# Performance work log

Hardware: AMD Instinct MI355X
Metric: run time of the kernel (lower is better)

## Reference

```python
import jax, jax.numpy as jnp
import numpy as np

B, N, D, K = 2, 8192, 512, 16


def setup_inputs() -> dict:
    key = jax.random.key(0)
    k1, k2, k3, k4 = jax.random.split(key, 4)
    x = jax.random.normal(k1, (B, N, D), dtype=jnp.float32)
    xyz = jax.random.normal(k2, (B, N, 3), dtype=jnp.float32)
    # nn.Linear(d_model, 3*d_model): weight [3D, D], bias [3D]
    W_qkv = jax.random.normal(k3, (3 * D, D), dtype=jnp.float32) * 0.02
    b_qkv = jnp.zeros((3 * D,), dtype=jnp.float32)
    # nn.Linear(d_model, d_model)
    W_fc = jax.random.normal(k4, (D, D), dtype=jnp.float32) * 0.02
    b_fc = jnp.zeros((D,), dtype=jnp.float32)
    return {"x": x, "xyz": xyz, "W_qkv": W_qkv, "b_qkv": b_qkv, "W_fc": W_fc, "b_fc": b_fc}


def _knn_idx(xyz):
    # squared-distance KNN (same ordering as cdist): |a|^2 + |b|^2 - 2 a.b
    sq = jnp.sum(xyz * xyz, axis=-1)                      # [B, N]
    d2 = sq[:, :, None] + sq[:, None, :] - 2.0 * jnp.einsum('bnc,bmc->bnm', xyz, xyz)
    return jax.lax.top_k(-d2, K)[1]                       # [B, N, K] smallest distances


def reference(x, xyz, W_qkv, b_qkv, W_fc, b_fc):
    knn_idx = _knn_idx(xyz)                               # no-grad in original
    qkv = jnp.einsum('bnd,ed->bne', x, W_qkv) + b_qkv     # [B, N, 3D]
    qkv = qkv.reshape(B, N, 3, D)
    q, k, v = qkv[:, :, 0], qkv[:, :, 1], qkv[:, :, 2]    # [B, N, D]
    gather = jax.vmap(lambda arr, idx: arr[idx])          # per-batch neighbor gather
    k_neigh = gather(k, knn_idx)                          # [B, N, K, D]
    v_neigh = gather(v, knn_idx)                          # [B, N, K, D]
    # faithful to einsum('bnd,bnsk->bns', q, k_neigh): sums d and feature dims independently
    attn = (q.sum(-1)[:, :, None] * k_neigh.sum(-1)) / jnp.sqrt(jnp.float32(D))  # [B, N, K]
    attn = jax.nn.softmax(attn, axis=2)[..., None]        # [B, N, K, 1]
    x_out = (attn * v_neigh).sum(axis=2)                  # [B, N, D]
    return jnp.einsum('bnd,ed->bne', x_out, W_fc) + b_fc + x
```

## Files before the change

kernel.cpp:

```cpp
#include <hip/hip_runtime.h>

typedef _Float16 half_t;
typedef _Float16 half8 __attribute__((ext_vector_type(8)));
typedef _Float16 half4v __attribute__((ext_vector_type(4)));
typedef float f32x4 __attribute__((ext_vector_type(4)));

#define NB 2
#define NN 8192
#define ND 512
#define NKNN 16
#define BN (NB*NN)

#define OFF_XH   0ull
#define OFF_VH   (OFF_XH  + (size_t)BN*ND*2)
#define OFF_XOH  (OFF_VH  + (size_t)BN*ND*2)
#define OFF_WVH  (OFF_XOH + (size_t)BN*ND*2)
#define OFF_WFCH (OFF_WVH + (size_t)ND*ND*2)
#define OFF_XW   (OFF_WFCH+ (size_t)ND*ND*2)
#define OFF_IDX  (OFF_XW  + (size_t)BN*16)
#define OFF_WQC  (OFF_IDX + (size_t)BN*NKNN*4)
#define OFF_WKC  (OFF_WQC + 2048)
#define OFF_QKB  (OFF_WKC + 2048)
#define OFF_QS   (OFF_QKB + 256)
#define OFF_KS   (OFF_QS  + (size_t)BN*4)

__global__ __launch_bounds__(256) void kcolsum(const float* __restrict__ W,
                                               float* __restrict__ wq,
                                               float* __restrict__ wk) {
  int h = blockIdx.x >> 3, g = blockIdx.x & 7;
  int t = threadIdx.x, dl = t & 63, s = t >> 6;
  const float* Wb = W + (size_t)h * 512 * 512;
  int d = g * 64 + dl;
  float acc = 0.f;
  for (int e = s * 128; e < s * 128 + 128; ++e) acc += Wb[(size_t)e * 512 + d];
  __shared__ float red[4][64];
  red[s][dl] = acc;
  __syncthreads();
  if (s == 0) (h ? wk : wq)[d] = red[0][dl] + red[1][dl] + red[2][dl] + red[3][dl];
}

__global__ __launch_bounds__(512) void kbias(const float* __restrict__ b,
                                             float* __restrict__ qkb) {
  __shared__ float r0[512], r1[512];
  int t = threadIdx.x;
  r0[t] = b[t]; r1[t] = b[512 + t];
  __syncthreads();
  for (int s = 256; s; s >>= 1) {
    if (t < s) { r0[t] += r0[t + s]; r1[t] += r1[t + s]; }
    __syncthreads();
  }
  if (t == 0) { qkb[0] = r0[0]; qkb[1] = r1[0]; }
}

__global__ __launch_bounds__(256) void kconvw(const float* __restrict__ wqkv,
                                              const float* __restrict__ wfc,
                                              half_t* __restrict__ wvh,
                                              half_t* __restrict__ wfch) {
  int i = blockIdx.x * 256 + threadIdx.x;
  float4 a = ((const float4*)(wqkv + 1024 * 512))[i];
  half4v ha; ha[0]=(half_t)a.x; ha[1]=(half_t)a.y; ha[2]=(half_t)a.z; ha[3]=(half_t)a.w;
  *(half4v*)(wvh + (size_t)i * 4) = ha;
  float4 c = ((const float4*)wfc)[i];
  half4v hc; hc[0]=(half_t)c.x; hc[1]=(half_t)c.y; hc[2]=(half_t)c.z; hc[3]=(half_t)c.w;
  *(half4v*)(wfch + (size_t)i * 4) = hc;
}

__global__ __launch_bounds__(256) void kxh(const float* __restrict__ x,
                                           const float* __restrict__ wq,
                                           const float* __restrict__ wk,
                                           const float* __restrict__ qkb,
                                           half_t* __restrict__ xh,
                                           float* __restrict__ qs,
                                           float* __restrict__ ks) {
  int wid = blockIdx.x * 4 + (threadIdx.x >> 6);
  int l = threadIdx.x & 63;
  size_t base = (size_t)wid * ND + l * 8;
  float4 a0 = *(const float4*)(x + base);
  float4 a1 = *(const float4*)(x + base + 4);
  half8 h;
  h[0]=(half_t)a0.x; h[1]=(half_t)a0.y; h[2]=(half_t)a0.z; h[3]=(half_t)a0.w;
  h[4]=(half_t)a1.x; h[5]=(half_t)a1.y; h[6]=(half_t)a1.z; h[7]=(half_t)a1.w;
  *(half8*)(xh + base) = h;
  float4 q0 = ((const float4*)(wq + l * 8))[0], q1 = ((const float4*)(wq + l * 8))[1];
  float4 k0 = ((const float4*)(wk + l * 8))[0], k1 = ((const float4*)(wk + l * 8))[1];
  float dq = a0.x*q0.x + a0.y*q0.y + a0.z*q0.z + a0.w*q0.w
           + a1.x*q1.x + a1.y*q1.y + a1.z*q1.z + a1.w*q1.w;
  float dk = a0.x*k0.x + a0.y*k0.y + a0.z*k0.z + a0.w*k0.w
           + a1.x*k1.x + a1.y*k1.y + a1.z*k1.z + a1.w*k1.w;
  #pragma unroll
  for (int o = 32; o; o >>= 1) { dq += __shfl_xor(dq, o); dk += __shfl_xor(dk, o); }
  if (l == 0) { qs[wid] = dq + qkb[0]; ks[wid] = dk + qkb[1]; }
}

__global__ __launch_bounds__(256) void kxyzw(const float* __restrict__ xyz,
                                             float4* __restrict__ xw) {
  int i = blockIdx.x * 256 + threadIdx.x;
  float ax = xyz[(size_t)i * 3 + 0], ay = xyz[(size_t)i * 3 + 1], az = xyz[(size_t)i * 3 + 2];
  float sq = __fadd_rn(__fadd_rn(__fmul_rn(ax, ax), __fmul_rn(ay, ay)), __fmul_rn(az, az));
  xw[i] = make_float4(ax, ay, az, sq);
}

#define QPW 4
__global__ __launch_bounds__(256) void kknn(const float4* __restrict__ xw,
                                            int* __restrict__ idxo) {
  __shared__ float4 tile[1024];
  const int tid = threadIdx.x;
  const int l = tid & 63;
  const int w = tid >> 6;
  const int b = blockIdx.x >> 9;
  const int qbase = (blockIdx.x & 511) * (4 * QPW) + w * QPW;
  const float4* xb = xw + (size_t)b * NN;

  float4 qp[QPW];
  #pragma unroll
  for (int qi = 0; qi < QPW; ++qi) qp[qi] = xb[qbase + qi];

  float mind[QPW]; int mini[QPW];
  #pragma unroll
  for (int qi = 0; qi < QPW; ++qi) { mind[qi] = __builtin_inff(); mini[qi] = 0x7fffffff; }

  for (int t = 0; t < 8; ++t) {
    __syncthreads();
    #pragma unroll
    for (int i = 0; i < 4; ++i) tile[i * 256 + tid] = xb[t * 1024 + i * 256 + tid];
    __syncthreads();
    #pragma unroll 4
    for (int it = 0; it < 16; ++it) {
      float4 cp = tile[it * 64 + l];
      int ci = t * 1024 + it * 64 + l;
      #pragma unroll
      for (int qi = 0; qi < QPW; ++qi) {
        float dot = fmaf(qp[qi].z, cp.z, fmaf(qp[qi].y, cp.y, __fmul_rn(qp[qi].x, cp.x)));
        float d2 = __fsub_rn(__fadd_rn(qp[qi].w, cp.w), __fmul_rn(2.0f, dot));
        if (d2 < mind[qi]) { mind[qi] = d2; mini[qi] = ci; }
      }
    }
  }

  float kd[QPW]; int ki[QPW]; float wst[QPW];
  #pragma unroll
  for (int qi = 0; qi < QPW; ++qi) {
    float d = mind[qi]; int ii = mini[qi];
    #pragma unroll
    for (int k = 2; k <= 64; k <<= 1) {
      #pragma unroll
      for (int j = k >> 1; j > 0; j >>= 1) {
        float od = __shfl_xor(d, j);
        int   oi = __shfl_xor(ii, j);
        bool up = ((l & k) == 0);
        bool lower_lane = ((l & j) == 0);
        bool oless = (od < d) || (od == d && oi < ii);
        bool take = (up == lower_lane) ? oless : !oless;
        if (take) { d = od; ii = oi; }
      }
    }
    kd[qi] = __shfl(d, l & 15);
    ki[qi] = __shfl(ii, l & 15);
    wst[qi] = __shfl(d, 15);
  }

  for (int t = 0; t < 8; ++t) {
    __syncthreads();
    #pragma unroll
    for (int i = 0; i < 4; ++i) tile[i * 256 + tid] = xb[t * 1024 + i * 256 + tid];
    __syncthreads();
    #pragma unroll 2
    for (int it = 0; it < 16; ++it) {
      float4 cp = tile[it * 64 + l];
      int ci = t * 1024 + it * 64 + l;
      #pragma unroll
      for (int qi = 0; qi < QPW; ++qi) {
        float dot = fmaf(qp[qi].z, cp.z, fmaf(qp[qi].y, cp.y, __fmul_rn(qp[qi].x, cp.x)));
        float d2 = __fsub_rn(__fadd_rn(qp[qi].w, cp.w), __fmul_rn(2.0f, dot));
        bool ok = (d2 <= wst[qi]) && (ci != mini[qi]);
        unsigned long long m = __ballot(ok);
        while (m) {
          int a = __builtin_ctzll(m);
          m &= m - 1;
          float dc = __shfl(d2, a);
          int ic = __shfl(ci, a);
          bool lower = (kd[qi] < dc) || (kd[qi] == dc && ki[qi] < ic);
          int r = __popcll(__ballot(lower) & 0xFFFFull);
          if (r < 16) {
            float pd = __shfl_up(kd[qi], 1, 16);
            int pi = __shfl_up(ki[qi], 1, 16);
            int p = l & 15;
            if (p == r)      { kd[qi] = dc; ki[qi] = ic; }
            else if (p > r)  { kd[qi] = pd; ki[qi] = pi; }
            wst[qi] = __shfl(kd[qi], 15, 16);
          }
        }
      }
    }
  }

  if (l < 16) {
    #pragma unroll
    for (int qi = 0; qi < QPW; ++qi)
      idxo[((size_t)b * NN + qbase + qi) * NKNN + l] = ki[qi];
  }
}

__device__ __forceinline__ void gload16(const void* g, void* l) {
  __builtin_amdgcn_global_load_lds((const __attribute__((address_space(1))) void*)g,
                                   (__attribute__((address_space(3))) void*)l, 16, 0, 0);
}

template <int EPI>
__global__ __launch_bounds__(256) void kgemm(const half_t* __restrict__ A,
                                             const half_t* __restrict__ Bw,
                                             const float* __restrict__ bias,
                                             const float* __restrict__ resid,
                                             void* __restrict__ Cout) {
  __shared__ __align__(16) half_t As[128 * 64];
  __shared__ __align__(16) half_t Bs[128 * 64];
  const int tid = threadIdx.x;
  const int l = tid & 63;
  const int w = tid >> 6;
  const int wm = w >> 1, wn = w & 1;
  const int mt = blockIdx.x >> 2;
  const int nt = blockIdx.x & 3;
  const int lr = l & 15, lg = l >> 4;

  f32x4 acc[4][4];
  #pragma unroll
  for (int i = 0; i < 4; ++i)
    #pragma unroll
    for (int j = 0; j < 4; ++j) acc[i][j] = (f32x4){0.f, 0.f, 0.f, 0.f};

  for (int kt = 0; kt < 8; ++kt) {
    #pragma unroll
    for (int i = 0; i < 4; ++i) {
      int id = i * 256 + tid;
      int rr = id >> 3, cc = id & 7;
      gload16(A + (size_t)(mt * 128 + rr) * ND + kt * 64 + cc * 8,
              (void*)(As + (size_t)(i * 256 + w * 64) * 8));
      gload16(Bw + (size_t)(nt * 128 + rr) * ND + kt * 64 + cc * 8,
              (void*)(Bs + (size_t)(i * 256 + w * 64) * 8));
    }
    __syncthreads();
    #pragma unroll
    for (int kk = 0; kk < 2; ++kk) {
      half8 af[4], bf[4];
      #pragma unroll
      for (int mi = 0; mi < 4; ++mi)
        af[mi] = *(const half8*)(As + (wm * 64 + mi * 16 + lr) * 64 + kk * 32 + lg * 8);
      #pragma unroll
      for (int ni = 0; ni < 4; ++ni)
        bf[ni] = *(const half8*)(Bs + (wn * 64 + ni * 16 + lr) * 64 + kk * 32 + lg * 8);
      #pragma unroll
      for (int mi = 0; mi < 4; ++mi)
        #pragma unroll
        for (int ni = 0; ni < 4; ++ni)
          acc[mi][ni] = __builtin_amdgcn_mfma_f32_16x16x32_f16(af[mi], bf[ni], acc[mi][ni], 0, 0, 0);
    }
    __syncthreads();
  }

  #pragma unroll
  for (int mi = 0; mi < 4; ++mi) {
    #pragma unroll
    for (int ni = 0; ni < 4; ++ni) {
      int col = nt * 128 + wn * 64 + ni * 16 + lr;
      #pragma unroll
      for (int r4 = 0; r4 < 4; ++r4) {
        size_t row = (size_t)mt * 128 + wm * 64 + mi * 16 + lg * 4 + r4;
        float v = acc[mi][ni][r4] + bias[col];
        if (EPI == 0) ((half_t*)Cout)[row * ND + col] = (half_t)v;
        else          ((float*)Cout)[row * ND + col] = v + resid[row * ND + col];
      }
    }
  }
}

__global__ __launch_bounds__(256) void kattn(const int* __restrict__ idx,
                                             const float* __restrict__ qs,
                                             const float* __restrict__ ks,
                                             const half_t* __restrict__ vh,
                                             half_t* __restrict__ xoh) {
  int wid = blockIdx.x * 4 + (threadIdx.x >> 6);
  int l = threadIdx.x & 63;
  int b = wid >> 13;
  int j = l & 15;
  int nb = idx[(size_t)wid * NKNN + j];
  float ksv = ks[(size_t)b * NN + nb];
  float logit = __fdiv_rn(__fmul_rn(qs[wid], ksv), 22.627416997969522f);
  float mx = logit;
  #pragma unroll
  for (int o = 8; o; o >>= 1) mx = fmaxf(mx, __shfl_xor(mx, o, 16));
  float e = expf(logit - mx);
  float s = e;
  #pragma unroll
  for (int o = 8; o; o >>= 1) s += __shfl_xor(s, o, 16);
  float p = e / s;

  float acc[8] = {0.f, 0.f, 0.f, 0.f, 0.f, 0.f, 0.f, 0.f};
  #pragma unroll
  for (int t16 = 0; t16 < 16; ++t16) {
    float wj = __shfl(p, t16, 16);
    int ij = __shfl(nb, t16, 16);
    const half8 vv = *(const half8*)(vh + ((size_t)b * NN + ij) * ND + l * 8);
    #pragma unroll
    for (int u = 0; u < 8; ++u) acc[u] += wj * (float)vv[u];
  }
  half8 ho;
  #pragma unroll
  for (int u = 0; u < 8; ++u) ho[u] = (half_t)acc[u];
  *(half8*)(xoh + (size_t)wid * ND + l * 8) = ho;
}

extern "C" void kernel_launch(void* const* d_in, const int* in_sizes, int n_in,
                              void* d_out, int out_size, void* d_ws, size_t ws_size,
                              hipStream_t stream) {
  const float* x    = (const float*)d_in[0];
  const float* xyz  = (const float*)d_in[1];
  const float* wqkv = (const float*)d_in[2];
  const float* bqkv = (const float*)d_in[3];
  const float* wfc  = (const float*)d_in[4];
  const float* bfc  = (const float*)d_in[5];
  char* ws = (char*)d_ws;
  half_t* xh   = (half_t*)(ws + OFF_XH);
  half_t* vh   = (half_t*)(ws + OFF_VH);
  half_t* xoh  = (half_t*)(ws + OFF_XOH);
  half_t* wvh  = (half_t*)(ws + OFF_WVH);
  half_t* wfch = (half_t*)(ws + OFF_WFCH);
  float4* xw   = (float4*)(ws + OFF_XW);
  int*    idx  = (int*)(ws + OFF_IDX);
  float*  wqc  = (float*)(ws + OFF_WQC);
  float*  wkc  = (float*)(ws + OFF_WKC);
  float*  qkb  = (float*)(ws + OFF_QKB);
  float*  qs   = (float*)(ws + OFF_QS);
  float*  ks   = (float*)(ws + OFF_KS);

  kcolsum<<<dim3(16),  dim3(256), 0, stream>>>(wqkv, wqc, wkc);
  kbias  <<<dim3(1),   dim3(512), 0, stream>>>(bqkv, qkb);
  kconvw <<<dim3(256), dim3(256), 0, stream>>>(wqkv, wfc, wvh, wfch);
  kxyzw  <<<dim3(64),  dim3(256), 0, stream>>>(xyz, xw);
  kxh    <<<dim3(4096),dim3(256), 0, stream>>>(x, wqc, wkc, qkb, xh, qs, ks);
  kknn   <<<dim3(1024),dim3(256), 0, stream>>>(xw, idx);
  kgemm<0><<<dim3(512),dim3(256), 0, stream>>>(xh, wvh, bqkv + 1024, (const float*)nullptr, (void*)vh);
  kattn  <<<dim3(4096),dim3(256), 0, stream>>>(idx, qs, ks, vh, xoh);
  kgemm<1><<<dim3(512),dim3(256), 0, stream>>>(xoh, wfch, bfc, x, d_out);
}
```

Before: 169.3 us.

## Pack candidate points in pairs for packed-FP32 KNN distance math

Adds a second point layout where each float4 holds coordinates of two adjacent points (x0,x1,y0,y1 and z0,z1,sq0,sq1). The KNN kernel then computes two candidate distances per lane with 2-wide float vector FMAs, which can map to packed FP32 instructions, and halves the inner-loop trip count. It also adds a min-blocks-per-CU launch bound. The distance formula changes from separate mul/sub rounding to a fused FMA with -2, which can alter tie ordering and neighbor selection slightly versus the reference.

```diff
diff --git a/kernel.cpp b/kernel.cpp
--- a/kernel.cpp
+++ b/kernel.cpp
@@ -4,6 +4,7 @@
 typedef _Float16 half8 __attribute__((ext_vector_type(8)));
 typedef _Float16 half4v __attribute__((ext_vector_type(4)));
 typedef float f32x4 __attribute__((ext_vector_type(4)));
+typedef float f32x2 __attribute__((ext_vector_type(2)));
 
 #define NB 2
 #define NN 8192
@@ -17,7 +18,8 @@
 #define OFF_WVH  (OFF_XOH + (size_t)BN*ND*2)
 #define OFF_WFCH (OFF_WVH + (size_t)ND*ND*2)
 #define OFF_XW   (OFF_WFCH+ (size_t)ND*ND*2)
-#define OFF_IDX  (OFF_XW  + (size_t)BN*16)
+#define OFF_XW2  (OFF_XW  + (size_t)BN*16)
+#define OFF_IDX  (OFF_XW2 + (size_t)BN*16)
 #define OFF_WQC  (OFF_IDX + (size_t)BN*NKNN*4)
 #define OFF_WKC  (OFF_WQC + 2048)
 #define OFF_QKB  (OFF_WKC + 2048)
@@ -93,27 +95,47 @@
 }
 
 __global__ __launch_bounds__(256) void kxyzw(const float* __restrict__ xyz,
-                                             float4* __restrict__ xw) {
-  int i = blockIdx.x * 256 + threadIdx.x;
-  float ax = xyz[(size_t)i * 3 + 0], ay = xyz[(size_t)i * 3 + 1], az = xyz[(size_t)i * 3 + 2];
-  float sq = __fadd_rn(__fadd_rn(__fmul_rn(ax, ax), __fmul_rn(ay, ay)), __fmul_rn(az, az));
-  xw[i] = make_float4(ax, ay, az, sq);
+                                             float4* __restrict__ xw,
+                                             float4* __restrict__ xw2) {
+  int p = blockIdx.x * 256 + threadIdx.x;
+  int b = p >> 12;
+  int pl = p & 4095;
+  int i0 = b * NN + pl * 2;
+  const float* s = xyz + (size_t)i0 * 3;
+  float x0 = s[0], y0 = s[1], z0 = s[2];
+  float x1 = s[3], y1 = s[4], z1 = s[5];
+  float sq0 = __fadd_rn(__fadd_rn(__fmul_rn(x0, x0), __fmul_rn(y0, y0)), __fmul_rn(z0, z0));
+  float sq1 = __fadd_rn(__fadd_rn(__fmul_rn(x1, x1), __fmul_rn(y1, y1)), __fmul_rn(z1, z1));
+  xw[i0]     = make_float4(x0, y0, z0, sq0);
+  xw[i0 + 1] = make_float4(x1, y1, z1, sq1);
+  xw2[(size_t)b * NN + pl]          = make_float4(x0, x1, y0, y1);
+  xw2[(size_t)b * NN + NN/2 + pl]   = make_float4(z0, z1, sq0, sq1);
 }
 
 #define QPW 4
-__global__ __launch_bounds__(256) void kknn(const float4* __restrict__ xw,
-                                            int* __restrict__ idxo) {
-  __shared__ float4 tile[1024];
+__global__ __launch_bounds__(256, 4) void kknn(const float4* __restrict__ xw,
+                                               const float4* __restrict__ xw2,
+                                               int* __restrict__ idxo) {
+  __shared__ __align__(16) float4 tile[1024];
   const int tid = threadIdx.x;
   const int l = tid & 63;
   const int w = tid >> 6;
   const int b = blockIdx.x >> 9;
   const int qbase = (blockIdx.x & 511) * (4 * QPW) + w * QPW;
-  const float4* xb = xw + (size_t)b * NN;
-
-  float4 qp[QPW];
-  #pragma unroll
-  for (int qi = 0; qi < QPW; ++qi) qp[qi] = xb[qbase + qi];
+  const float4* xb  = xw  + (size_t)b * NN;
+  const float4* xa2 = xw2 + (size_t)b * NN;
+  const float4* xb2 = xa2 + NN / 2;
+
+  f32x2 qxx[QPW], qyy[QPW], qzz[QPW], qww[QPW];
+  #pragma unroll
+  for (int qi = 0; qi < QPW; ++qi) {
+    float4 qp = xb[qbase + qi];
+    qxx[qi] = (f32x2){qp.x, qp.x};
+    qyy[qi] = (f32x2){qp.y, qp.y};
+    qzz[qi] = (f32x2){qp.z, qp.z};
+    qww[qi] = (f32x2){qp.w, qp.w};
+  }
+  const f32x2 m2 = (f32x2){-2.0f, -2.0f};
 
   float mind[QPW]; int mini[QPW];
   #pragma unroll
@@ -121,18 +143,29 @@
 
   for (int t = 0; t < 8; ++t) {
     __syncthreads();
-    #pragma unroll
-    for (int i = 0; i < 4; ++i) tile[i * 256 + tid] = xb[t * 1024 + i * 256 + tid];
-    __syncthreads();
-    #pragma unroll 4
-    for (int it = 0; it < 16; ++it) {
-      float4 cp = tile[it * 64 + l];
-      int ci = t * 1024 + it * 64 + l;
+    tile[tid]       = xa2[t * 512 + tid];
+    tile[256 + tid] = xa2[t * 512 + 256 + tid];
+    tile[512 + tid] = xb2[t * 512 + tid];
+    tile[768 + tid] = xb2[t * 512 + 256 + tid];
+    __syncthreads();
+    #pragma unroll
+    for (int it = 0; it < 8; ++it) {
+      int p = it * 64 + l;
+      float4 A = tile[p];
+      float4 Bv = tile[512 + p];
+      f32x2 cx = (f32x2){A.x, A.y};
+      f32x2 cy = (f32x2){A.z, A.w};
+      f32x2 cz = (f32x2){Bv.x, Bv.y};
+      f32x2 cw = (f32x2){Bv.z, Bv.w};
+      int ci0 = t * 1024 + p * 2;
       #pragma unroll
       for (int qi = 0; qi < QPW; ++qi) {
-        float dot = fmaf(qp[qi].z, cp.z, fmaf(qp[qi].y, cp.y, __fmul_rn(qp[qi].x, cp.x)));
-        float d2 = __fsub_rn(__fadd_rn(qp[qi].w, cp.w), __fmul_rn(2.0f, dot));
-        if (d2 < mind[qi]) { mind[qi] = d2; mini[qi] = ci; }
+        f32x2 dot = __builtin_elementwise_fma(qzz[qi], cz,
+                      __builtin_elementwise_fma(qyy[qi], cy, qxx[qi] * cx));
+        f32x2 s2 = qww[qi] + cw;
+        f32x2 d2 = __builtin_elementwise_fma(m2, dot, s2);
+        if (d2.x < mind[qi]) { mind[qi] = d2.x; mini[qi] = ci0; }
+        if (d2.y < mind[qi]) { mind[qi] = d2.y; mini[qi] = ci0 + 1; }
       }
     }
   }
@@ -159,37 +192,53 @@
     wst[qi] = __shfl(d, 15);
   }
 
+  auto insert = [&](bool ok, float dv, int iv, int qi) {
+    unsigned long long m = __ballot(ok);
+    while (m) {
+      int a = __builtin_ctzll(m);
+      m &= m - 1;
+      float dc = __shfl(dv, a);
+      int ic = __shfl(iv, a);
+      bool lower = (kd[qi] < dc) || (kd[qi] == dc && ki[qi] < ic);
+      int r = __popcll(__ballot(lower) & 0xFFFFull);
+      if (r < 16) {
+        float pd = __shfl_up(kd[qi], 1, 16);
+        int pi = __shfl_up(ki[qi], 1, 16);
+        int pp = l & 15;
+        if (pp == r)      { kd[qi] = dc; ki[qi] = ic; }
+        else if (pp > r)  { kd[qi] = pd; ki[qi] = pi; }
+        wst[qi] = __shfl(kd[qi], 15, 16);
+      }
+    }
+  };
+
   for (int t = 0; t < 8; ++t) {
     __syncthreads();
-    #pragma unroll
-    for (int i = 0; i < 4; ++i) tile[i * 256 + tid] = xb[t * 1024 + i * 256 + tid];
+    tile[tid]       = xa2[t * 512 + tid];
+    tile[256 + tid] = xa2[t * 512 + 256 + tid];
+    tile[512 + tid] = xb2[t * 512 + tid];
+    tile[768 + tid] = xb2[t * 512 + 256 + tid];
     __syncthreads();
     #pragma unroll 2
-    for (int it = 0; it < 16; ++it) {
-      float4 cp = tile[it * 64 + l];
-      int ci = t * 1024 + it * 64 + l;
+    for (int it = 0; it < 8; ++it) {
+      int p = it * 64 + l;
+      float4 A = tile[p];
+      float4 Bv = tile[512 + p];
+      f32x2 cx = (f32x2){A.x, A.y};
+      f32x2 cy = (f32x2){A.z, A.w};
+      f32x2 cz = (f32x2){Bv.x, Bv.y};
+      f32x2 cw = (f32x2){Bv.z, Bv.w};
+      int ci0 = t * 1024 + p * 2;
       #pragma unroll
       for (int qi = 0; qi < QPW; ++qi) {
-        float dot = fmaf(qp[qi].z, cp.z, fmaf(qp[qi].y, cp.y, __fmul_rn(qp[qi].x, cp.x)));
-        float d2 = __fsub_rn(__fadd_rn(qp[qi].w, cp.w), __fmul_rn(2.0f, dot));
-        bool ok = (d2 <= wst[qi]) && (ci != mini[qi]);
-        unsigned long long m = __ballot(ok);
-        while (m) {
-          int a = __builtin_ctzll(m);
-          m &= m - 1;
-          float dc = __shfl(d2, a);
-          int ic = __shfl(ci, a);
-          bool lower = (kd[qi] < dc) || (kd[qi] == dc && ki[qi] < ic);
-          int r = __popcll(__ballot(lower) & 0xFFFFull);
-          if (r < 16) {
-            float pd = __shfl_up(kd[qi], 1, 16);
-            int pi = __shfl_up(ki[qi], 1, 16);
-            int p = l & 15;
-            if (p == r)      { kd[qi] = dc; ki[qi] = ic; }
-            else if (p > r)  { kd[qi] = pd; ki[qi] = pi; }
-            wst[qi] = __shfl(kd[qi], 15, 16);
-          }
-        }
+        f32x2 dot = __builtin_elementwise_fma(qzz[qi], cz,
+                      __builtin_elementwise_fma(qyy[qi], cy, qxx[qi] * cx));
+        f32x2 s2 = qww[qi] + cw;
+        f32x2 d2 = __builtin_elementwise_fma(m2, dot, s2);
+        bool ok0 = (d2.x <= wst[qi]) && (ci0 != mini[qi]);
+        bool ok1 = (d2.y <= wst[qi]) && (ci0 + 1 != mini[qi]);
+        insert(ok0, d2.x, ci0, qi);
+        insert(ok1, d2.y, ci0 + 1, qi);
       }
     }
   }
@@ -325,6 +374,7 @@
   half_t* wvh  = (half_t*)(ws + OFF_WVH);
   half_t* wfch = (half_t*)(ws + OFF_WFCH);
   float4* xw   = (float4*)(ws + OFF_XW);
+  float4* xw2  = (float4*)(ws + OFF_XW2);
   int*    idx  = (int*)(ws + OFF_IDX);
   float*  wqc  = (float*)(ws + OFF_WQC);
   float*  wkc  = (float*)(ws + OFF_WKC);
@@ -335,9 +385,9 @@
   kcolsum<<<dim3(16),  dim3(256), 0, stream>>>(wqkv, wqc, wkc);
   kbias  <<<dim3(1),   dim3(512), 0, stream>>>(bqkv, qkb);
   kconvw <<<dim3(256), dim3(256), 0, stream>>>(wqkv, wfc, wvh, wfch);
-  kxyzw  <<<dim3(64),  dim3(256), 0, stream>>>(xyz, xw);
+  kxyzw  <<<dim3(32),  dim3(256), 0, stream>>>(xyz, xw, xw2);
   kxh    <<<dim3(4096),dim3(256), 0, stream>>>(x, wqc, wkc, qkb, xh, qs, ks);
-  kknn   <<<dim3(1024),dim3(256), 0, stream>>>(xw, idx);
+  kknn   <<<dim3(1024),dim3(256), 0, stream>>>(xw, xw2, idx);
   kgemm<0><<<dim3(512),dim3(256), 0, stream>>>(xh, wvh, bqkv + 1024, (const float*)nullptr, (void*)vh);
   kattn  <<<dim3(4096),dim3(256), 0, stream>>>(idx, qs, ks, vh, xoh);
   kgemm<1><<<dim3(512),dim3(256), 0, stream>>>(xoh, wfch, bfc, x, d_out);
```

Result: no change. 168.6 us (-0.4%).
